# Performance work log

Hardware: AMD Instinct MI355X
Metric: run time of the kernel (lower is better)

The kernel has to match this reference:

```python
import jax, jax.numpy as jnp
import numpy as np

B, H, W, C = 32, 56, 56, 256
HEADS, WS, SS, MLP = 8, 7, 3, 1024
N = WS * WS          # tokens per window = 49
HD = C // HEADS      # head dim = 32
SCALE = HD ** -0.5
EPS = 1e-5


def _rel_pos_index():
    coords = np.stack(np.meshgrid(np.arange(WS), np.arange(WS), indexing='ij')).reshape(2, -1)
    rel = (coords[:, :, None] - coords[:, None, :]).transpose(1, 2, 0)
    rel[:, :, 0] += WS - 1
    rel[:, :, 1] += WS - 1
    rel[:, :, 0] *= 2 * WS - 1
    return rel.sum(-1)  # (49, 49) int


def _shift_mask():
    ma = np.zeros((H, W), np.float32)
    sl = (slice(0, -WS), slice(-WS, -SS), slice(-SS, None))
    cnt = 0
    for hs in sl:
        for ws_ in sl:
            ma[hs, ws_] = cnt
            cnt += 1
    mw = ma.reshape(H // WS, WS, W // WS, WS).transpose(0, 2, 1, 3).reshape(-1, N)
    diff = mw[:, None, :] - mw[:, :, None]
    return np.where(diff != 0, np.float32(-100.0), np.float32(0.0))  # (nW, 49, 49)


_RPI = _rel_pos_index()
_MASK = jnp.asarray(_shift_mask())


def _ln(x, g, b):
    mu = jnp.mean(x, -1, keepdims=True)
    var = jnp.mean(jnp.square(x - mu), -1, keepdims=True)
    return (x - mu) * jax.lax.rsqrt(var + EPS) * g + b


def setup_inputs() -> dict:
    key = jax.random.key(0)
    ks = jax.random.split(key, 6)
    s = 0.02
    return {
        'x': jax.random.normal(ks[0], (B, H * W, C), jnp.float32),
        'qkv_w': jax.random.normal(ks[1], (C, 3 * C), jnp.float32) * s,
        'qkv_b': jnp.zeros((3 * C,), jnp.float32),
        'proj_w': jax.random.normal(ks[2], (C, C), jnp.float32) * s,
        'proj_b': jnp.zeros((C,), jnp.float32),
        'rel_bias': jax.random.normal(ks[3], ((2 * WS - 1) ** 2, HEADS), jnp.float32) * s,
        'ln1_g': jnp.ones((C,), jnp.float32),
        'ln1_b': jnp.zeros((C,), jnp.float32),
        'ln2_g': jnp.ones((C,), jnp.float32),
        'ln2_b': jnp.zeros((C,), jnp.float32),
        'mlp_w1': jax.random.normal(ks[4], (C, MLP), jnp.float32) * s,
        'mlp_b1': jnp.zeros((MLP,), jnp.float32),
        'mlp_w2': jax.random.normal(ks[5], (MLP, C), jnp.float32) * s,
        'mlp_b2': jnp.zeros((C,), jnp.float32),
    }


def reference(x, qkv_w, qkv_b, proj_w, proj_b, rel_bias,
              ln1_g, ln1_b, ln2_g, ln2_b, mlp_w1, mlp_b1, mlp_w2, mlp_b2):
    b = x.shape[0]
    nW = (H // WS) * (W // WS)

    x_skip = x
    xn = _ln(x, ln1_g, ln1_b).reshape(b, H, W, C)
    shifted = jnp.roll(xn, (-SS, -SS), axis=(1, 2))
    # window partition -> (b*nW, N, C)
    xw = shifted.reshape(b, H // WS, WS, W // WS, WS, C)
    xw = xw.transpose(0, 1, 3, 2, 4, 5).reshape(-1, N, C)

    qkv = (xw @ qkv_w + qkv_b).reshape(-1, N, 3, HEADS, HD).transpose(2, 0, 3, 1, 4)
    q, k, v = qkv[0] * SCALE, qkv[1], qkv[2]  # (b*nW, heads, N, hd)

    attn = jnp.einsum('bhnd,bhmd->bhnm', q, k)
    bias = rel_bias[_RPI.reshape(-1)].reshape(N, N, HEADS).transpose(2, 0, 1)
    attn = attn + bias[None]
    attn = attn.reshape(b, nW, HEADS, N, N) + _MASK[None, :, None]
    attn = jax.nn.softmax(attn.reshape(-1, HEADS, N, N), axis=-1)

    out = jnp.einsum('bhnm,bhmd->bhnd', attn, v)
    out = out.transpose(0, 2, 1, 3).reshape(-1, N, C)
    out = out @ proj_w + proj_b

    # window reverse -> (b, H, W, C)
    out = out.reshape(b, H // WS, W // WS, WS, WS, C)
    out = out.transpose(0, 1, 3, 2, 4, 5).reshape(b, H, W, C)
    out = jnp.roll(out, (SS, SS), axis=(1, 2)).reshape(b, H * W, C)

    x = x_skip + out
    x_skip2 = x
    xn2 = _ln(x, ln2_g, ln2_b)
    h = jax.nn.gelu(xn2 @ mlp_w1 + mlp_b1, approximate=False)
    h = h @ mlp_w2 + mlp_b2
    return x_skip2 + h
```

## Files before the change

kernel.cpp:

```cpp
#include <hip/hip_runtime.h>


typedef unsigned short u16;
typedef __attribute__((ext_vector_type(8))) short bfrag8;
typedef __attribute__((ext_vector_type(8))) unsigned short u16x8;
typedef __attribute__((ext_vector_type(4))) float f32x4;

#define WS_TOK 49
#define C_DIM 256
#define M_ROWS 100352
#define N_WIN 2048
#define SCALE_Q 0.17677669529663689f

#if defined(__has_builtin)
#  if __has_builtin(__builtin_amdgcn_global_load_lds)
#    define HAVE_GLL 1
#  endif
#endif
#ifndef HAVE_GLL
#  define HAVE_GLL 0
#endif

__device__ __forceinline__ float u2f(u16 u) {
    union { unsigned int i; float f; } c; c.i = ((unsigned int)u) << 16; return c.f;
}
__device__ __forceinline__ u16 f2u(float f) {
    union { float f; unsigned int i; } c; c.f = f;
    unsigned int i = c.i;
    return (u16)((i + 0x7fffu + ((i >> 16) & 1u)) >> 16);
}
__device__ __forceinline__ int regionOf(int h) {
    return h < 49 ? 0 : (h < 53 ? 1 : 2);
}
__device__ __forceinline__ float gelu_tanh(float v) {
    const float y = 0.79788456080286536f * (v + 0.044715f * v * v * v);
    const float e = __expf(2.f * y);
    const float t = 1.f - 2.f / (e + 1.f);
    return 0.5f * v * (1.f + t);
}

__device__ __forceinline__ void g2l16(const u16* g, u16* l) {
#if HAVE_GLL
    __builtin_amdgcn_global_load_lds((const __attribute__((address_space(1))) void*)g,
                                     (__attribute__((address_space(3))) void*)l, 16, 0, 0);
#else
    *(bfrag8*)l = *(const bfrag8*)g;
#endif
}

__global__ void transpose_k(const float* __restrict__ in, u16* __restrict__ out,
                            int R, int Ccols) {
    int i = blockIdx.x * 256 + threadIdx.x;
    if (i < R * Ccols) {
        int r = i / Ccols, c = i - r * Ccols;
        out[(size_t)c * R + r] = f2u(in[i]);
    }
}

__global__ __launch_bounds__(256) void ln_kernel(const float* __restrict__ xin,
                                                 const float* __restrict__ g,
                                                 const float* __restrict__ b,
                                                 u16* __restrict__ out, int mode) {
    const int w = threadIdx.x >> 6, lane = threadIdx.x & 63;
    const int r = blockIdx.x * 4 + w;
    int s = r;
    if (mode == 0) {
        const int win = r / WS_TOK, tok = r - win * WS_TOK;
        const int b_ = win >> 6, w64 = win & 63;
        const int wr = w64 >> 3, wc = w64 & 7;
        const int th = tok / 7, tw = tok - th * 7;
        int hh = wr * 7 + th + 3; if (hh >= 56) hh -= 56;
        int ww = wc * 7 + tw + 3; if (ww >= 56) ww -= 56;
        s = b_ * 3136 + hh * 56 + ww;
    }
    const float4 u = *(const float4*)(xin + (size_t)s * C_DIM + lane * 4);
    float f0 = u.x, f1 = u.y, f2 = u.z, f3 = u.w;
    float s1 = f0 + f1 + f2 + f3;
    float s2 = f0 * f0 + f1 * f1 + f2 * f2 + f3 * f3;
#pragma unroll
    for (int off = 32; off; off >>= 1) {
        s1 += __shfl_xor(s1, off, 64);
        s2 += __shfl_xor(s2, off, 64);
    }
    const float mu = s1 * (1.f / 256.f);
    const float rs = rsqrtf(s2 * (1.f / 256.f) - mu * mu + 1e-5f);
    const float4 ug = *(const float4*)(g + lane * 4);
    const float4 ub = *(const float4*)(b + lane * 4);
    ushort4 o;
    o.x = f2u((f0 - mu) * rs * ug.x + ub.x);
    o.y = f2u((f1 - mu) * rs * ug.y + ub.y);
    o.z = f2u((f2 - mu) * rs * ug.z + ub.z);
    o.w = f2u((f3 - mu) * rs * ug.w + ub.w);
    *(ushort4*)(out + (size_t)r * C_DIM + lane * 4) = o;
}

template <int KD, int ND, int NY, int EPI>
__global__ __launch_bounds__(256) void gemm_bt(const u16* __restrict__ A,
                                               const u16* __restrict__ Bt,
                                               const float* __restrict__ bias,
                                               u16* __restrict__ o0,
                                               u16* __restrict__ o1,
                                               u16* __restrict__ o2,
                                               float* __restrict__ fo,
                                               const float* __restrict__ res) {
    __shared__ __align__(16) char pool[17408];
    u16* As = (u16*)pool;
    u16* Bs = (u16*)(pool + 8192);
    const int tid = threadIdx.x;
    const int bid = blockIdx.x;
    const int m0 = (bid / NY) * 128;
    const int n0 = (bid % NY) * 128;
    const int wid = tid >> 6, lane = tid & 63;
    const int wy = wid >> 1, wx = wid & 1;
    const int l15 = lane & 15, lsel = lane >> 4;

    f32x4 acc[4][4] = {};
    const u16* Ag = A + (size_t)m0 * KD;
    const u16* Bg = Bt + (size_t)n0 * KD;

    for (int k0 = 0; k0 < KD; k0 += 32) {
#pragma unroll
        for (int p = 0; p < 2; ++p) {
            const int idx = p * 256 + tid;
            const int row = idx >> 2, ks = (idx & 3) << 3;
            g2l16(Ag + (size_t)row * KD + k0 + ks, As + idx * 8);
            g2l16(Bg + (size_t)row * KD + k0 + ks, Bs + idx * 8);
        }
        __syncthreads();
        bfrag8 af[4], bfv[4];
#pragma unroll
        for (int m = 0; m < 4; ++m)
            af[m] = *(const bfrag8*)(As + (wy * 64 + m * 16 + l15) * 32 + lsel * 8);
#pragma unroll
        for (int n = 0; n < 4; ++n)
            bfv[n] = *(const bfrag8*)(Bs + (wx * 64 + n * 16 + l15) * 32 + lsel * 8);
#pragma unroll
        for (int m = 0; m < 4; ++m)
#pragma unroll
            for (int n = 0; n < 4; ++n)
                acc[m][n] = __builtin_amdgcn_mfma_f32_16x16x32_bf16(af[m], bfv[n],
                                                                    acc[m][n], 0, 0, 0);
        __syncthreads();
    }

    float* Ts = (float*)pool + wid * (16 * 68);
    const int r  = lane >> 2;
    const int cg = (lane & 3) << 4;

#pragma unroll
    for (int m = 0; m < 4; ++m) {
#pragma unroll
        for (int n = 0; n < 4; ++n)
#pragma unroll
            for (int reg = 0; reg < 4; ++reg)
                Ts[(lsel * 4 + reg) * 68 + n * 16 + l15] = acc[m][n][reg];
        float vals[16];
#pragma unroll
        for (int j = 0; j < 4; ++j)
            *(f32x4*)(vals + 4 * j) = *(const f32x4*)(Ts + r * 68 + cg + 4 * j);

        const int gr  = m0 + wy * 64 + m * 16 + r;
        const int gc0 = n0 + wx * 64 + cg;
        float bias16[16];
#pragma unroll
        for (int j = 0; j < 4; ++j)
            *(f32x4*)(bias16 + 4 * j) = *(const f32x4*)(bias + gc0 + 4 * j);

        if (EPI == 0) {
            const int win = gr / WS_TOK, tok = gr - win * WS_TOK;
            const int part = gc0 >> 8, head = (gc0 >> 5) & 7, hd = gc0 & 31;
            u16* dst = (part == 0) ? o0 : (part == 1) ? o1 : o2;
            const float sc = (part == 0) ? SCALE_Q : 1.f;
            const size_t di = (size_t)win * 8 * (WS_TOK * 32) + (size_t)tok * 32 +
                              (size_t)head * (WS_TOK * 32) + hd;
            u16x8 pk[2];
#pragma unroll
            for (int j = 0; j < 16; ++j)
                ((u16*)pk)[j] = f2u((vals[j] + bias16[j]) * sc);
            *(u16x8*)(dst + di)     = pk[0];
            *(u16x8*)(dst + di + 8) = pk[1];
        } else if (EPI == 1) {
            const int win = gr / WS_TOK, tok = gr - win * WS_TOK;
            const int b_ = win >> 6, w64 = win & 63;
            const int wr = w64 >> 3, wc = w64 & 7;
            const int th = tok / 7, tw = tok - th * 7;
            int hh = wr * 7 + th + 3; if (hh >= 56) hh -= 56;
            int ww = wc * 7 + tw + 3; if (ww >= 56) ww -= 56;
            const size_t di = ((size_t)b_ * 3136 + hh * 56 + ww) * C_DIM + gc0;
#pragma unroll
            for (int j = 0; j < 4; ++j) {
                f32x4 rr = *(const f32x4*)(res + di + 4 * j);
                f32x4 o;
#pragma unroll
                for (int e = 0; e < 4; ++e)
                    o[e] = rr[e] + vals[4 * j + e] + bias16[4 * j + e];
                *(f32x4*)(fo + di + 4 * j) = o;
            }
        } else if (EPI == 2) {
            u16x8 pk[2];
#pragma unroll
            for (int j = 0; j < 16; ++j)
                ((u16*)pk)[j] = f2u(gelu_tanh(vals[j] + bias16[j]));
            u16* dst = o0 + (size_t)gr * ND + gc0;
            *(u16x8*)dst       = pk[0];
            *(u16x8*)(dst + 8) = pk[1];
        } else {
            const size_t di = (size_t)gr * ND + gc0;
#pragma unroll
            for (int j = 0; j < 4; ++j) {
                f32x4 rr = *(const f32x4*)(res + di + 4 * j);
                f32x4 o;
#pragma unroll
                for (int e = 0; e < 4; ++e)
                    o[e] = rr[e] + vals[4 * j + e] + bias16[4 * j + e];
                *(f32x4*)(fo + di + 4 * j) = o;
            }
        }
    }
}

__global__ __launch_bounds__(256) void attn_kernel(const u16* __restrict__ q,
                                                   const u16* __restrict__ k,
                                                   const u16* __restrict__ v,
                                                   const float* __restrict__ relb,
                                                   u16* __restrict__ ao) {
    __shared__ __align__(16) u16 PbAll[4][64 * 64];
    __shared__ __align__(16) u16 VtAll[4][32 * 64];
    const int wid = threadIdx.x >> 6;
    const int lane = threadIdx.x & 63;
    u16* Pb = PbAll[wid];
    u16* Vt = VtAll[wid];
    const int bid = blockIdx.x * 4 + wid;
    const int head = bid & 7, win = bid >> 3;
    const int w64 = win & 63;
    const int wr = w64 >> 3, wc = w64 & 7;
    const int l15 = lane & 15, lsel = lane >> 4;
    const size_t base = (size_t)bid * (WS_TOK * 32);
    const u16* qb = q + base;
    const u16* kb = k + base;
    const u16* vb = v + base;

    for (int idx = lane; idx < WS_TOK * 32; idx += 64) {
        const int tok = idx >> 5, dim = idx & 31;
        Vt[dim * 64 + tok] = vb[idx];
    }
    for (int i = lane; i < 32 * 15; i += 64) {
        const int dim = i / 15, tok = 49 + (i - dim * 15);
        Vt[dim * 64 + tok] = 0;
    }

    bfrag8 qf[4], kf[4];
#pragma unroll
    for (int m = 0; m < 4; ++m) {
        int tok = m * 16 + l15; if (tok > 48) tok = 48;
        qf[m] = *(const bfrag8*)(qb + tok * 32 + lsel * 8);
    }
#pragma unroll
    for (int n = 0; n < 4; ++n) {
        int tok = n * 16 + l15; if (tok > 48) tok = 48;
        kf[n] = *(const bfrag8*)(kb + tok * 32 + lsel * 8);
    }
    f32x4 S[4][4] = {};
#pragma unroll
    for (int m = 0; m < 4; ++m)
#pragma unroll
        for (int n = 0; n < 4; ++n)
            S[m][n] = __builtin_amdgcn_mfma_f32_16x16x32_bf16(qf[m], kf[n], S[m][n], 0, 0, 0);

#pragma unroll
    for (int m = 0; m < 4; ++m) {
#pragma unroll
        for (int reg = 0; reg < 4; ++reg) {
            const int row = m * 16 + lsel * 4 + reg;
            const int rowc = row > 48 ? 48 : row;
            const int ih = rowc / 7, iw = rowc - ih * 7;
            const int ri = regionOf(wr * 7 + ih) * 3 + regionOf(wc * 7 + iw);
            float sv[4];
#pragma unroll
            for (int n = 0; n < 4; ++n) {
                const int col = n * 16 + l15;
                float val = S[m][n][reg];
                if (col > 48) {
                    val = -1e30f;
                } else {
                    const int jh = col / 7, jw = col - jh * 7;
                    val += relb[((ih - jh + 6) * 13 + (iw - jw + 6)) * 8 + head];
                    const int rj = regionOf(wr * 7 + jh) * 3 + regionOf(wc * 7 + jw);
                    if (ri != rj) val -= 100.f;
                }
                sv[n] = val;
            }
            float mx = fmaxf(fmaxf(sv[0], sv[1]), fmaxf(sv[2], sv[3]));
#pragma unroll
            for (int off = 1; off < 16; off <<= 1) mx = fmaxf(mx, __shfl_xor(mx, off, 64));
            float p[4], sum = 0.f;
#pragma unroll
            for (int n = 0; n < 4; ++n) { p[n] = __expf(sv[n] - mx); sum += p[n]; }
#pragma unroll
            for (int off = 1; off < 16; off <<= 1) sum += __shfl_xor(sum, off, 64);
            const float inv = 1.f / sum;
#pragma unroll
            for (int n = 0; n < 4; ++n)
                Pb[row * 64 + n * 16 + l15] = f2u(p[n] * inv);
        }
    }

    f32x4 O[4][2] = {};
    bfrag8 vf[2][2];
#pragma unroll
    for (int n = 0; n < 2; ++n) {
        vf[n][0] = *(const bfrag8*)(Vt + (n * 16 + l15) * 64 + lsel * 8);
        vf[n][1] = *(const bfrag8*)(Vt + (n * 16 + l15) * 64 + 32 + lsel * 8);
    }
#pragma unroll
    for (int m = 0; m < 4; ++m) {
        const bfrag8 pf0 = *(const bfrag8*)(Pb + (m * 16 + l15) * 64 + lsel * 8);
        const bfrag8 pf1 = *(const bfrag8*)(Pb + (m * 16 + l15) * 64 + 32 + lsel * 8);
#pragma unroll
        for (int n = 0; n < 2; ++n) {
            O[m][n] = __builtin_amdgcn_mfma_f32_16x16x32_bf16(pf0, vf[n][0], O[m][n], 0, 0, 0);
            O[m][n] = __builtin_amdgcn_mfma_f32_16x16x32_bf16(pf1, vf[n][1], O[m][n], 0, 0, 0);
        }
    }
    const size_t aob = (size_t)win * (WS_TOK * C_DIM) + head * 32;
#pragma unroll
    for (int m = 0; m < 4; ++m) {
#pragma unroll
        for (int reg = 0; reg < 4; ++reg) {
            const int row = m * 16 + lsel * 4 + reg;
            if (row < WS_TOK) {
#pragma unroll
                for (int n = 0; n < 2; ++n)
                    ao[aob + (size_t)row * C_DIM + n * 16 + l15] = f2u(O[m][n][reg]);
            }
        }
    }
}

extern "C" void kernel_launch(void* const* d_in, const int* in_sizes, int n_in,
                              void* d_out, int out_size, void* d_ws, size_t ws_size,
                              hipStream_t stream) {
    (void)in_sizes; (void)n_in; (void)out_size; (void)ws_size;
    const float* x      = (const float*)d_in[0];
    const float* qkv_w  = (const float*)d_in[1];
    const float* qkv_b  = (const float*)d_in[2];
    const float* proj_w = (const float*)d_in[3];
    const float* proj_b = (const float*)d_in[4];
    const float* relb   = (const float*)d_in[5];
    const float* ln1g   = (const float*)d_in[6];
    const float* ln1b   = (const float*)d_in[7];
    const float* ln2g   = (const float*)d_in[8];
    const float* ln2b   = (const float*)d_in[9];
    const float* w1     = (const float*)d_in[10];
    const float* b1     = (const float*)d_in[11];
    const float* w2     = (const float*)d_in[12];
    const float* b2     = (const float*)d_in[13];
    float* out = (float*)d_out;

    const size_t SZ = (size_t)M_ROWS * C_DIM;
    u16* wsu  = (u16*)d_ws;
    u16* xw   = wsu;
    u16* qq   = wsu + SZ;
    u16* kk   = wsu + 2 * SZ;
    u16* vv   = wsu + 3 * SZ;
    u16* ao   = wsu + 4 * SZ;
    u16* z    = xw;
    u16* h    = qq;
    u16* qkvT = wsu + 5 * SZ;
    u16* projT = qkvT + 256 * 768;
    u16* w1T  = projT + 256 * 256;
    u16* w2T  = w1T + 256 * 1024;

    transpose_k<<<768, 256, 0, stream>>>(qkv_w, qkvT, 256, 768);
    transpose_k<<<256, 256, 0, stream>>>(proj_w, projT, 256, 256);
    transpose_k<<<1024, 256, 0, stream>>>(w1, w1T, 256, 1024);
    transpose_k<<<1024, 256, 0, stream>>>(w2, w2T, 1024, 256);

    ln_kernel<<<M_ROWS / 4, 256, 0, stream>>>(x, ln1g, ln1b, xw, 0);

    gemm_bt<256, 768, 6, 0><<<784 * 6, 256, 0, stream>>>(xw, qkvT, qkv_b,
                                                         qq, kk, vv, nullptr, nullptr);

    attn_kernel<<<N_WIN * 8 / 4, 256, 0, stream>>>(qq, kk, vv, relb, ao);

    gemm_bt<256, 256, 2, 1><<<784 * 2, 256, 0, stream>>>(ao, projT, proj_b,
                                                         nullptr, nullptr, nullptr, out, x);

    ln_kernel<<<M_ROWS / 4, 256, 0, stream>>>(out, ln2g, ln2b, z, 1);

    gemm_bt<256, 1024, 8, 2><<<784 * 8, 256, 0, stream>>>(z, w1T, b1,
                                                          h, nullptr, nullptr, nullptr, nullptr);

    gemm_bt<1024, 256, 2, 3><<<784 * 2, 256, 0, stream>>>(h, w2T, b2,
                                                          nullptr, nullptr, nullptr, out, out);
}
```

Before: 794.3 us.

## Fuse MLP fc1, GELU and fc2 into one kernel keeping hidden tile in LDS

Replaces the two MLP GEMM launches with a single kernel that processes 64 rows at a time. It computes 128-column chunks of the hidden activation, applies bias and GELU, stores the chunk in LDS, and immediately accumulates it into the fc2 output. This removes the write and reread of the large bf16 hidden tensor through global memory. In exchange each block reloads the z tile for every hidden chunk and keeps large accumulators in registers, which lowers occupancy. It also uses only 1568 blocks with modest MFMA tiles and no pipelining of loads against compute.

```diff
diff --git a/kernel.cpp b/kernel.cpp
--- a/kernel.cpp
+++ b/kernel.cpp
@@ -217,6 +217,134 @@
             }
         }
     }
+}
+
+__global__ __launch_bounds__(256, 2) void fused_mlp(const u16* __restrict__ z,
+                                                    const u16* __restrict__ w1T,
+                                                    const float* __restrict__ b1,
+                                                    const u16* __restrict__ w2T,
+                                                    const float* __restrict__ b2,
+                                                    float* __restrict__ out) {
+    __shared__ __align__(16) u16 pool[20480];
+    u16* sA  = pool;
+    u16* sB1 = pool + 4096;
+    u16* sB2 = pool;
+    u16* hc  = pool + 12288;
+    const int tid = threadIdx.x;
+    const int wid = tid >> 6, lane = tid & 63;
+    const int wy = wid >> 1, wx = wid & 1;
+    const int l15 = lane & 15, lsel = lane >> 4;
+    const int m0 = blockIdx.x * 64;
+
+    f32x4 acc2[2][8] = {};
+
+    for (int kc = 0; kc < 8; ++kc) {
+        f32x4 acc1[2][4] = {};
+        const u16* w1c = w1T + ((size_t)kc << 7) * 256;
+        for (int k0 = 0; k0 < 256; k0 += 64) {
+#pragma unroll
+            for (int p = 0; p < 2; ++p) {
+                const int i = p * 256 + tid;
+                const int row = i >> 3, s = i & 7;
+                g2l16(z + (size_t)(m0 + row) * 256 + k0 + ((s ^ (row & 7)) << 3),
+                      sA + i * 8);
+            }
+#pragma unroll
+            for (int p = 0; p < 4; ++p) {
+                const int i = p * 256 + tid;
+                const int row = i >> 3, s = i & 7;
+                g2l16(w1c + (size_t)row * 256 + k0 + ((s ^ (row & 7)) << 3),
+                      sB1 + i * 8);
+            }
+            __syncthreads();
+#pragma unroll
+            for (int sub = 0; sub < 2; ++sub) {
+                bfrag8 af[2], bf[4];
+#pragma unroll
+                for (int m = 0; m < 2; ++m) {
+                    const int r = wy * 32 + m * 16 + l15;
+                    af[m] = *(const bfrag8*)(sA + r * 64 +
+                             ((sub * 32 + lsel * 8) ^ ((r & 7) << 3)));
+                }
+#pragma unroll
+                for (int n = 0; n < 4; ++n) {
+                    const int r = wx * 64 + n * 16 + l15;
+                    bf[n] = *(const bfrag8*)(sB1 + r * 64 +
+                             ((sub * 32 + lsel * 8) ^ ((r & 7) << 3)));
+                }
+#pragma unroll
+                for (int m = 0; m < 2; ++m)
+#pragma unroll
+                    for (int n = 0; n < 4; ++n)
+                        acc1[m][n] = __builtin_amdgcn_mfma_f32_16x16x32_bf16(
+                            af[m], bf[n], acc1[m][n], 0, 0, 0);
+            }
+            __syncthreads();
+        }
+        float b1v[4];
+#pragma unroll
+        for (int n = 0; n < 4; ++n)
+            b1v[n] = b1[(kc << 7) + wx * 64 + n * 16 + l15];
+#pragma unroll
+        for (int m = 0; m < 2; ++m)
+#pragma unroll
+            for (int n = 0; n < 4; ++n)
+#pragma unroll
+                for (int reg = 0; reg < 4; ++reg) {
+                    const int rh = wy * 32 + m * 16 + lsel * 4 + reg;
+                    const int ch = wx * 64 + n * 16 + l15;
+                    hc[rh * 128 + (ch ^ ((rh & 15) << 3))] =
+                        f2u(gelu_tanh(acc1[m][n][reg] + b1v[n]));
+                }
+
+        for (int ks = 0; ks < 4; ++ks) {
+#pragma unroll
+            for (int p = 0; p < 4; ++p) {
+                const int i = p * 256 + tid;
+                const int n = i >> 2, s = i & 3;
+                g2l16(w2T + (size_t)n * 1024 + (kc << 7) + ks * 32 +
+                          ((s ^ ((n >> 1) & 3)) << 3),
+                      sB2 + i * 8);
+            }
+            __syncthreads();
+            bfrag8 a2[2], bb[8];
+#pragma unroll
+            for (int m = 0; m < 2; ++m) {
+                const int r = wy * 32 + m * 16 + l15;
+                a2[m] = *(const bfrag8*)(hc + r * 128 +
+                         ((ks * 32 + lsel * 8) ^ ((r & 15) << 3)));
+            }
+#pragma unroll
+            for (int n = 0; n < 8; ++n) {
+                const int r = wx * 128 + n * 16 + l15;
+                bb[n] = *(const bfrag8*)(sB2 + r * 32 +
+                         ((lsel * 8) ^ (((r >> 1) & 3) << 3)));
+            }
+#pragma unroll
+            for (int m = 0; m < 2; ++m)
+#pragma unroll
+                for (int n = 0; n < 8; ++n)
+                    acc2[m][n] = __builtin_amdgcn_mfma_f32_16x16x32_bf16(
+                        a2[m], bb[n], acc2[m][n], 0, 0, 0);
+            __syncthreads();
+        }
+    }
+
+    float b2v[8];
+#pragma unroll
+    for (int n = 0; n < 8; ++n)
+        b2v[n] = b2[wx * 128 + n * 16 + l15];
+#pragma unroll
+    for (int m = 0; m < 2; ++m)
+#pragma unroll
+        for (int reg = 0; reg < 4; ++reg) {
+            const int row = m0 + wy * 32 + m * 16 + lsel * 4 + reg;
+#pragma unroll
+            for (int n = 0; n < 8; ++n) {
+                const size_t di = (size_t)row * 256 + wx * 128 + n * 16 + l15;
+                out[di] += acc2[m][n][reg] + b2v[n];
+            }
+        }
 }
 
 __global__ __launch_bounds__(256) void attn_kernel(const u16* __restrict__ q,
@@ -365,7 +493,6 @@
     u16* vv   = wsu + 3 * SZ;
     u16* ao   = wsu + 4 * SZ;
     u16* z    = xw;
-    u16* h    = qq;
     u16* qkvT = wsu + 5 * SZ;
     u16* projT = qkvT + 256 * 768;
     u16* w1T  = projT + 256 * 256;
@@ -388,9 +515,5 @@
 
     ln_kernel<<<M_ROWS / 4, 256, 0, stream>>>(out, ln2g, ln2b, z, 1);
 
-    gemm_bt<256, 1024, 8, 2><<<784 * 8, 256, 0, stream>>>(z, w1T, b1,
-                                                          h, nullptr, nullptr, nullptr, nullptr);
-
-    gemm_bt<1024, 256, 2, 3><<<784 * 2, 256, 0, stream>>>(h, w2T, b2,
-                                                          nullptr, nullptr, nullptr, out, out);
-}
+    fused_mlp<<<M_ROWS / 64, 256, 0, stream>>>(z, w1T, b1, w2T, b2, out);
+}
```

Result: faster. 768.4 us (-3.3%).
